# Kernel optimization log

Measured on AMD Instinct MI355X. Metric: run time of the kernel, lower is better.

The kernel has to match this reference:

```python
import jax, jax.numpy as jnp
import numpy as np

HEAD_SIZE = 64

def setup_inputs() -> dict:
    key = jax.random.key(0)
    k1, k2, k3, k4 = jax.random.split(key, 4)
    B, T, C = 4, 4096, 768
    s = 1.0 / np.sqrt(C)
    return {
        "x": jax.random.normal(k1, (B, T, C), dtype=jnp.float32),
        "Wq": jax.random.normal(k2, (C, HEAD_SIZE), dtype=jnp.float32) * s,
        "Wk": jax.random.normal(k3, (C, HEAD_SIZE), dtype=jnp.float32) * s,
        "Wv": jax.random.normal(k4, (C, HEAD_SIZE), dtype=jnp.float32) * s,
    }

def reference(x, Wq, Wk, Wv):
    # x: [B,T,C]; Wq/Wk/Wv: [C,H]
    T = x.shape[1]
    q = jnp.einsum('btc,ch->bth', x, Wq)
    k = jnp.einsum('btc,ch->bth', x, Wk)
    v = jnp.einsum('btc,ch->bth', x, Wv)
    scale = HEAD_SIZE ** (-0.5)
    wei = jnp.einsum('bth,bsh->bts', q, k) * scale  # [B,T,T]
    causal = jnp.tril(jnp.ones((T, T), dtype=bool))
    wei = jnp.where(causal, wei, -jnp.inf)
    wei = jax.nn.softmax(wei, axis=-1)
    # dropout p=0.0 -> identity
    out = jnp.einsum('bts,bsh->bth', wei, v)  # [B,T,H]
    return out
```

## Files before the change

### kernel.cpp

```cpp
#include <hip/hip_runtime.h>
#include <hip/hip_bf16.h>
#include <stdint.h>
#include <math.h>

typedef unsigned short u16;
typedef __attribute__((ext_vector_type(8))) __bf16 bf16x8;
typedef __attribute__((ext_vector_type(4))) float f32x4;

#define LOG2E 1.44269504088896340736f

__device__ inline u16 f2bf(float f){
  uint32_t u = __float_as_uint(f);
  u += 0x7FFFu + ((u >> 16) & 1u);
  return (u16)(u >> 16);
}
__device__ inline float bf2f(u16 v){
  return __uint_as_float(((uint32_t)v) << 16);
}

typedef const __attribute__((address_space(1))) void* gas_t;
typedef __attribute__((address_space(3))) void* las_t;
__device__ inline void gl_lds16(const void* g, void* l){
  __builtin_amdgcn_global_load_lds((gas_t)g, (las_t)l, 16, 0, 0);
}

__global__ __launch_bounds__(256) void wt_kernel(const float* __restrict__ Wq,
                                                 const float* __restrict__ Wk,
                                                 const float* __restrict__ Wv,
                                                 u16* __restrict__ wtf){
  int idx = blockIdx.x * 256 + threadIdx.x;
  if (idx >= 192 * 768) return;
  int n = idx / 768, c = idx - n * 768;
  int h = n & 63;
  const float* W = (n < 64) ? Wq : ((n < 128) ? Wk : Wv);
  float v = W[c * 64 + h];
  if (n < 64) v *= 0.125f * LOG2E;
  int f = n >> 4, n16 = n & 15;
  int kstep = c >> 5, quad = (c >> 3) & 3, j = c & 7;
  wtf[(size_t)((f * 24 + kstep) * 64 + quad * 16 + n16) * 8 + j] = f2bf(v);
}

__global__ __launch_bounds__(256) void proj_kernel(const float* __restrict__ x,
                                                   const u16* __restrict__ wtf,
                                                   u16* __restrict__ qs,
                                                   u16* __restrict__ ksf,
                                                   u16* __restrict__ vtf){
  __shared__ u16 At[24 * 64 * 8];
  const int tid = threadIdx.x;
  const int w = tid >> 6, lane = tid & 63;
  const int n16 = lane & 15, quad = lane >> 4;
  const int rt = blockIdx.x * 16;

  const float* xb = x + (size_t)rt * 768;
  float4 t[12];
#pragma unroll
  for (int i = 0; i < 12; ++i)
    t[i] = *(const float4*)(xb + (size_t)(i * 256 + tid) * 4);
#pragma unroll
  for (int i = 0; i < 12; ++i){
    int l = i * 256 + tid;
    int row = l / 192, c4 = l - row * 192;
    int ksn = c4 >> 3, qd = (c4 >> 1) & 3, j0 = (c4 & 1) * 4;
    int idx = ((ksn * 64 + qd * 16 + row) * 8 + j0) ^ ((ksn & 7) << 3);
    union { ushort4 s; u16 e[4]; } pk;
    pk.e[0] = f2bf(t[i].x); pk.e[1] = f2bf(t[i].y);
    pk.e[2] = f2bf(t[i].z); pk.e[3] = f2bf(t[i].w);
    *(ushort4*)&At[idx] = pk.s;
  }
  __syncthreads();

  const f32x4 fz = {0.f, 0.f, 0.f, 0.f};
  f32x4 acc[3];
#pragma unroll
  for (int j = 0; j < 3; ++j) acc[j] = fz;

#pragma unroll
  for (int kst = 0; kst < 24; ++kst){
    const int sw = (kst & 7) << 3;
    bf16x8 a = *(const bf16x8*)&At[((kst * 64 + lane) * 8) ^ sw];
#pragma unroll
    for (int j = 0; j < 3; ++j){
      bf16x8 bfr = *(const bf16x8*)(wtf + (size_t)(((3 * w + j) * 24 + kst) * 64 + lane) * 8);
      acc[j] = __builtin_amdgcn_mfma_f32_16x16x32_bf16(a, bfr, acc[j], 0, 0, 0);
    }
  }
  __syncthreads();

#pragma unroll
  for (int j = 0; j < 3; ++j){
    const int F = 3 * w + j;
    const int s = F >> 2, c0 = (F & 3) * 16;
#pragma unroll
    for (int r = 0; r < 4; ++r){
      u16 val = f2bf(acc[j][r]);
      int row = quad * 4 + r;
      if (s < 2) At[s * 1152 + row * 72 + c0 + n16] = val;
      else       At[2304 + (c0 + n16) * 24 + row]   = val;
    }
  }
  __syncthreads();

  const int bb = rt >> 12, t0 = rt & 4095;
  const int kt = t0 >> 6;
  const int fk = (t0 >> 4) & 3;
  const int half0 = (t0 >> 5) & 1;
  const int qhalf = (t0 >> 4) & 1;
  if (tid < 128){
    int row = tid >> 3, hc = tid & 7;
    uint4 qv = *(const uint4*)&At[row * 72 + hc * 8];
    *(uint4*)(qs + (size_t)(rt + row) * 64 + hc * 8) = qv;
  } else {
    int tt = tid - 128;
    int half = tt >> 6, l2 = tt & 63;
    int nn = l2 & 15, qq = l2 >> 4;
    uint4 kv = *(const uint4*)&At[1152 + nn * 72 + half * 32 + qq * 8];
    size_t off = ((((size_t)(bb * 64 + kt) * 4 + fk) * 2 + half) * 64 + l2) * 8;
    *(uint4*)(ksf + off) = kv;
  }
  if (tid < 128){
    int f = tid >> 5, idx5 = tid & 31;
    int qsel = idx5 >> 4, nn = idx5 & 15;
    int h = f * 16 + nn;
    uint4 vv = *(const uint4*)&At[2304 + h * 24 + qsel * 8];
    int lane2 = (2 * qhalf + qsel) * 16 + nn;
    size_t off = ((((size_t)(bb * 64 + kt) * 4 + f) * 2 + half0) * 64 + lane2) * 8;
    *(uint4*)(vtf + off) = vv;
  }
}

__global__ __launch_bounds__(256) void flash_part(const u16* __restrict__ qs,
                                                  const u16* __restrict__ ksf,
                                                  const u16* __restrict__ vtf,
                                                  u16* __restrict__ Opart,
                                                  float* __restrict__ ml){
  const int gid = blockIdx.x;
  int b, qt, ck, nt;
  if (gid < 1024){
    b = gid >> 8;
    int r = gid & 255;
    int m = (int)sqrtf((float)r);
    if (m * m > r) --m;
    if ((m + 1) * (m + 1) <= r) ++m;
    int d = r - m * m;
    if (d < m){ qt = 2 * m;     ck = d;     }
    else      { qt = 2 * m + 1; ck = d - m; }
    nt = 4;
  } else {
    int t = gid - 1024;
    b = t >> 4;
    int m = t & 15;
    qt = 2 * m; ck = m; nt = 2;
  }
  const int kt0 = ck * 4;

  __shared__ u16 Kb[4096];
  __shared__ u16 Vb[4096];
  __shared__ u16 Ps[128 * 72];
  const int tid = threadIdx.x;
  const int w = tid >> 6, lane = tid & 63;
  const int n16 = lane & 15, quad = lane >> 4;

  const u16* qb  = qs  + (size_t)b * 262144;
  const u16* kpg = ksf + (size_t)b * 262144 + (size_t)kt0 * 4096;
  const u16* vpg = vtf + (size_t)b * 262144 + (size_t)kt0 * 4096;

  bf16x8 qA[2][2];
#pragma unroll
  for (int m = 0; m < 2; ++m){
    const size_t qrow = (size_t)(qt * 128 + w * 32 + m * 16 + n16) * 64;
    qA[m][0] = *(const bf16x8*)(qb + qrow + quad * 8);
    qA[m][1] = *(const bf16x8*)(qb + qrow + 32 + quad * 8);
  }

  const f32x4 fz = {0.f, 0.f, 0.f, 0.f};
  f32x4 O[2][4];
  float rs[2][4];
#pragma unroll
  for (int m = 0; m < 2; ++m)
#pragma unroll
    for (int f = 0; f < 4; ++f){ O[m][f] = fz; rs[m][f] = 0.f; }

#define STAGE(ti)                                                            \
  {                                                                          \
    const u16* kg = kpg + (size_t)(ti) * 4096 + (w * 2) * 512 + lane * 8;    \
    const u16* vg = vpg + (size_t)(ti) * 4096 + (w * 2) * 512 + lane * 8;    \
    gl_lds16(kg,       &Kb[(w * 2 + 0) * 512]);                              \
    gl_lds16(kg + 512, &Kb[(w * 2 + 1) * 512]);                              \
    gl_lds16(vg,       &Vb[(w * 2 + 0) * 512]);                              \
    gl_lds16(vg + 512, &Vb[(w * 2 + 1) * 512]);                              \
  }

  for (int it = 0; it < nt; ++it){
    const int kt = kt0 + it;
    if (it) __syncthreads();
    STAGE(it);
    __syncthreads();

    f32x4 S[2][4];
#pragma unroll
    for (int f = 0; f < 4; ++f){
      bf16x8 k0 = *(const bf16x8*)&Kb[(f * 2 + 0) * 512 + lane * 8];
      bf16x8 k1 = *(const bf16x8*)&Kb[(f * 2 + 1) * 512 + lane * 8];
#pragma unroll
      for (int m = 0; m < 2; ++m){
        f32x4 s = fz;
        s = __builtin_amdgcn_mfma_f32_16x16x32_bf16(qA[m][0], k0, s, 0, 0, 0);
        s = __builtin_amdgcn_mfma_f32_16x16x32_bf16(qA[m][1], k1, s, 0, 0, 0);
        S[m][f] = s;
      }
    }

    if (kt >= 2 * qt){
#pragma unroll
      for (int m = 0; m < 2; ++m)
#pragma unroll
        for (int f = 0; f < 4; ++f)
#pragma unroll
          for (int r = 0; r < 4; ++r){
            int col = kt * 64 + f * 16 + n16;
            int row = qt * 128 + w * 32 + m * 16 + quad * 4 + r;
            if (col > row) S[m][f][r] = -1e30f;
          }
    }

#pragma unroll
    for (int m = 0; m < 2; ++m)
#pragma unroll
      for (int f = 0; f < 4; ++f)
#pragma unroll
        for (int r = 0; r < 4; ++r){
          float p = __builtin_amdgcn_exp2f(S[m][f][r]);
          S[m][f][r] = p;
          rs[m][r] += p;
        }

#pragma unroll
    for (int m = 0; m < 2; ++m)
#pragma unroll
      for (int f = 0; f < 4; ++f){
        u16* p = &Ps[(w * 32 + m * 16 + quad * 4) * 72 + f * 16 + n16];
        p[0]   = f2bf(S[m][f][0]);
        p[72]  = f2bf(S[m][f][1]);
        p[144] = f2bf(S[m][f][2]);
        p[216] = f2bf(S[m][f][3]);
      }
    bf16x8 pA[2][2];
#pragma unroll
    for (int m = 0; m < 2; ++m){
      pA[m][0] = *(const bf16x8*)&Ps[(w * 32 + m * 16 + n16) * 72 + quad * 8];
      pA[m][1] = *(const bf16x8*)&Ps[(w * 32 + m * 16 + n16) * 72 + 32 + quad * 8];
    }

#pragma unroll
    for (int f = 0; f < 4; ++f){
      bf16x8 v0 = *(const bf16x8*)&Vb[(f * 2 + 0) * 512 + lane * 8];
      bf16x8 v1 = *(const bf16x8*)&Vb[(f * 2 + 1) * 512 + lane * 8];
#pragma unroll
      for (int m = 0; m < 2; ++m){
        O[m][f] = __builtin_amdgcn_mfma_f32_16x16x32_bf16(pA[m][0], v0, O[m][f], 0, 0, 0);
        O[m][f] = __builtin_amdgcn_mfma_f32_16x16x32_bf16(pA[m][1], v1, O[m][f], 0, 0, 0);
      }
    }
  }
#undef STAGE

#pragma unroll
  for (int m = 0; m < 2; ++m)
#pragma unroll
    for (int r = 0; r < 4; ++r){
#pragma unroll
      for (int off = 1; off < 16; off <<= 1)
        rs[m][r] += __shfl_xor(rs[m][r], off, 16);
    }

  const size_t oidx = (size_t)gid * 8192;
#pragma unroll
  for (int m = 0; m < 2; ++m)
#pragma unroll
    for (int f = 0; f < 4; ++f)
#pragma unroll
      for (int r = 0; r < 4; ++r){
        int row_local = w * 32 + m * 16 + quad * 4 + r;
        Opart[oidx + (size_t)row_local * 64 + f * 16 + n16] = f2bf(O[m][f][r]);
      }
  if (n16 == 0){
    float* lp = ml + (size_t)gid * 128;
#pragma unroll
    for (int m = 0; m < 2; ++m)
#pragma unroll
      for (int r = 0; r < 4; ++r)
        lp[w * 32 + m * 16 + quad * 4 + r] = rs[m][r];
  }
}

__global__ __launch_bounds__(256) void combine_kernel(const u16* __restrict__ Opart,
                                                      const float* __restrict__ ml,
                                                      float* __restrict__ out){
  const int gid = blockIdx.x * 256 + threadIdx.x;
  const int bq = gid >> 11;
  const int rem = (gid & 2047) * 4;
  const int row = rem >> 6;
  const int b = bq >> 5, qt = bq & 31;
  const int m = qt >> 1;
  const int nc4 = (qt & 1) ? (m + 1) : m;
  const int F = (qt & 1) ? (m * m + m) : (m * m);

  float L = 0.f;
  float a0 = 0.f, a1 = 0.f, a2 = 0.f, a3 = 0.f;
  for (int j = 0; j < nc4; ++j){
    int p = b * 256 + F + j;
    L += ml[(size_t)p * 128 + row];
    const u16* q = Opart + (size_t)p * 8192 + rem;
    uint2 d = *(const uint2*)q;
    a0 += bf2f((u16)(d.x & 0xffffu));
    a1 += bf2f((u16)(d.x >> 16));
    a2 += bf2f((u16)(d.y & 0xffffu));
    a3 += bf2f((u16)(d.y >> 16));
  }
  if (!(qt & 1)){
    int p = 1024 + b * 16 + m;
    L += ml[(size_t)p * 128 + row];
    const u16* q = Opart + (size_t)p * 8192 + rem;
    uint2 d = *(const uint2*)q;
    a0 += bf2f((u16)(d.x & 0xffffu));
    a1 += bf2f((u16)(d.x >> 16));
    a2 += bf2f((u16)(d.y & 0xffffu));
    a3 += bf2f((u16)(d.y >> 16));
  }
  const float invL = 1.0f / L;
  float4 v = {a0 * invL, a1 * invL, a2 * invL, a3 * invL};
  *(float4*)(out + (size_t)gid * 4) = v;
}

extern "C" void kernel_launch(void* const* d_in, const int* in_sizes, int n_in,
                              void* d_out, int out_size, void* d_ws, size_t ws_size,
                              hipStream_t stream){
  const float* x  = (const float*)d_in[0];
  const float* Wq = (const float*)d_in[1];
  const float* Wk = (const float*)d_in[2];
  const float* Wv = (const float*)d_in[3];
  float* out = (float*)d_out;

  u16* qs  = (u16*)d_ws;
  u16* ksf = qs  + (size_t)16384 * 64;
  u16* vtf = ksf + (size_t)16384 * 64;
  u16* wtf = vtf + (size_t)16384 * 64;
  u16* Opart = wtf + (size_t)192 * 768;
  float* ml = (float*)(Opart + (size_t)1088 * 8192);

  wt_kernel<<<576, 256, 0, stream>>>(Wq, Wk, Wv, wtf);
  proj_kernel<<<1024, 256, 0, stream>>>(x, wtf, qs, ksf, vtf);
  flash_part<<<1088, 256, 0, stream>>>(qs, ksf, vtf, Opart, ml);
  combine_kernel<<<1024, 256, 0, stream>>>(Opart, ml, out);
}
```

Measured before the change: 131.1 us.

## Prefetch K/V tiles into registers one iteration ahead instead of direct LDS loads

```diff
diff --git a/kernel.cpp b/kernel.cpp
--- a/kernel.cpp
+++ b/kernel.cpp
@@ -16,12 +16,6 @@
 }
 __device__ inline float bf2f(u16 v){
   return __uint_as_float(((uint32_t)v) << 16);
-}
-
-typedef const __attribute__((address_space(1))) void* gas_t;
-typedef __attribute__((address_space(3))) void* las_t;
-__device__ inline void gl_lds16(const void* g, void* l){
-  __builtin_amdgcn_global_load_lds((gas_t)g, (las_t)l, 16, 0, 0);
 }
 
 __global__ __launch_bounds__(256) void wt_kernel(const float* __restrict__ Wq,
@@ -180,21 +174,27 @@
 #pragma unroll
     for (int f = 0; f < 4; ++f){ O[m][f] = fz; rs[m][f] = 0.f; }
 
-#define STAGE(ti)                                                            \
+  uint4 rk0, rk1, rv0, rv1;
+#define LOADR(ti)                                                            \
   {                                                                          \
-    const u16* kg = kpg + (size_t)(ti) * 4096 + (w * 2) * 512 + lane * 8;    \
-    const u16* vg = vpg + (size_t)(ti) * 4096 + (w * 2) * 512 + lane * 8;    \
-    gl_lds16(kg,       &Kb[(w * 2 + 0) * 512]);                              \
-    gl_lds16(kg + 512, &Kb[(w * 2 + 1) * 512]);                              \
-    gl_lds16(vg,       &Vb[(w * 2 + 0) * 512]);                              \
-    gl_lds16(vg + 512, &Vb[(w * 2 + 1) * 512]);                              \
-  }
+    const u16* kg = kpg + (size_t)(ti) * 4096 + tid * 16;                    \
+    const u16* vg = vpg + (size_t)(ti) * 4096 + tid * 16;                    \
+    rk0 = *(const uint4*)kg;  rk1 = *(const uint4*)(kg + 8);                 \
+    rv0 = *(const uint4*)vg;  rv1 = *(const uint4*)(vg + 8);                 \
+  }
+#define WRITES()                                                             \
+  {                                                                          \
+    *(uint4*)&Kb[tid * 16] = rk0;  *(uint4*)&Kb[tid * 16 + 8] = rk1;         \
+    *(uint4*)&Vb[tid * 16] = rv0;  *(uint4*)&Vb[tid * 16 + 8] = rv1;         \
+  }
+
+  LOADR(0);
+  WRITES();
+  if (nt > 1) LOADR(1);
+  __syncthreads();
 
   for (int it = 0; it < nt; ++it){
     const int kt = kt0 + it;
-    if (it) __syncthreads();
-    STAGE(it);
-    __syncthreads();
 
     f32x4 S[2][4];
 #pragma unroll
@@ -261,8 +261,16 @@
         O[m][f] = __builtin_amdgcn_mfma_f32_16x16x32_bf16(pA[m][1], v1, O[m][f], 0, 0, 0);
       }
     }
-  }
-#undef STAGE
+
+    if (it + 1 < nt){
+      __syncthreads();
+      WRITES();
+      if (it + 2 < nt) LOADR(it + 2);
+      __syncthreads();
+    }
+  }
+#undef LOADR
+#undef WRITES
 
 #pragma unroll
   for (int m = 0; m < 2; ++m)
```

After: 129.2 us. Within noise of the previous version (-1.4%).
